# Kernel optimization log

Hardware: AMD Instinct MI355X
Metric: run time of the kernel (lower is better)

Reference implementation:

```python
import jax, jax.numpy as jnp
import numpy as np
import math

EMBED_DIM = 2048
NUM_HEADS = 16
HEAD_DIM = EMBED_DIM // NUM_HEADS  # 128
B, T, S_CACHE = 32, 16, 8192


def setup_inputs() -> dict:
    key = jax.random.key(0)
    ks = jax.random.split(key, 8)
    sc = 0.02
    return {
        "x": jax.random.normal(ks[0], (B, T, EMBED_DIM), dtype=jnp.float32),
        "K_cache": jax.random.normal(ks[1], (B, 1, S_CACHE, HEAD_DIM), dtype=jnp.float32),
        "V_cache": jax.random.normal(ks[2], (B, 1, S_CACHE, HEAD_DIM), dtype=jnp.float32),
        "Wq": jax.random.normal(ks[3], (EMBED_DIM, EMBED_DIM), dtype=jnp.float32) * sc,
        "bq": jnp.zeros((EMBED_DIM,), dtype=jnp.float32),
        "Wk": jax.random.normal(ks[4], (HEAD_DIM, EMBED_DIM), dtype=jnp.float32) * sc,
        "bk": jnp.zeros((HEAD_DIM,), dtype=jnp.float32),
        "Wv": jax.random.normal(ks[5], (HEAD_DIM, EMBED_DIM), dtype=jnp.float32) * sc,
        "bv": jnp.zeros((HEAD_DIM,), dtype=jnp.float32),
        "Wo": jax.random.normal(ks[6], (EMBED_DIM, EMBED_DIM), dtype=jnp.float32) * sc,
        "bo": jnp.zeros((EMBED_DIM,), dtype=jnp.float32),
    }


def reference(x, K_cache, V_cache, Wq, bq, Wk, bk, Wv, bv, Wo, bo):
    b, t, d = x.shape
    # projections (nn.Linear: x @ W.T + b)
    Q = (x @ Wq.T + bq).reshape(b, t, NUM_HEADS, HEAD_DIM).transpose(0, 2, 1, 3)  # [B,H,T,hd]
    K_new = (x @ Wk.T + bk)[:, None, :, :]  # [B,1,T,hd]
    V_new = (x @ Wv.T + bv)[:, None, :, :]
    K = jnp.concatenate([K_cache, K_new], axis=2)  # [B,1,S,hd]
    V = jnp.concatenate([V_cache, V_new], axis=2)
    scale = 1.0 / math.sqrt(HEAD_DIM)
    # shared single KV head broadcast across query heads
    att = jnp.einsum('bhtd,bsd->bhts', Q, K[:, 0]) * scale  # [B,H,T,S]
    att = jax.nn.softmax(att, axis=-1)
    out = jnp.einsum('bhts,bsd->bhtd', att, V[:, 0])  # [B,H,T,hd]
    out = out.transpose(0, 2, 1, 3).reshape(b, t, d)
    out = out @ Wo.T + bo  # dropout is identity in eval mode
    return out
```

## Files before the change

### kernel.cpp

```cpp
#include <hip/hip_runtime.h>
#include <cstdint>

#define EMB 2048
#define NH 16
#define HD 128
#define BB 32
#define TT 16
#define SC 8192
#define ST 8208
#define NS 8
#define QK_SCALE 0.08838834764831845f

typedef __attribute__((ext_vector_type(8))) short short8;
typedef __attribute__((ext_vector_type(4))) float f32x4;

__device__ __forceinline__ ushort f2bf(float f) {
  union { float f; uint32_t u; } v; v.f = f;
  uint32_t u = v.u;
  return (ushort)((u + 0x7FFFu + ((u >> 16) & 1u)) >> 16);
}

typedef __attribute__((address_space(1))) void gas_t;
typedef __attribute__((address_space(3))) void las_t;
__device__ __forceinline__ void gload16(const void* g, void* l) {
  __builtin_amdgcn_global_load_lds((gas_t*)g, (las_t*)l, 16, 0, 0);
}

__global__ __launch_bounds__(256) void prepack(
    const float* __restrict__ x, const float* __restrict__ Wq,
    const float* __restrict__ Wk, const float* __restrict__ Wv,
    const float* __restrict__ Wo, const float* __restrict__ bq,
    const float* __restrict__ bk, const float* __restrict__ bv,
    ushort* __restrict__ xbf, ushort* __restrict__ wqkv,
    ushort* __restrict__ wobf, float* __restrict__ biasq) {
  const int B0 = 262144;
  const int B1 = B0 + 1048576;
  const int B2 = B1 + 65536;
  const int B3 = B2 + 65536;
  const int B4 = B3 + 1048576;
  const int B5 = B4 + 576;
  int stride = gridDim.x * blockDim.x;
  for (int i = blockIdx.x * blockDim.x + threadIdx.x; i < B5; i += stride) {
    const float* src; ushort* dst;
    if (i < B0)      { src = x  + (size_t)i * 4;        dst = xbf  + (size_t)i * 4; }
    else if (i < B1) { src = Wq + (size_t)(i - B0) * 4; dst = wqkv + (size_t)(i - B0) * 4; }
    else if (i < B2) { src = Wk + (size_t)(i - B1) * 4; dst = wqkv + 4194304 + (size_t)(i - B1) * 4; }
    else if (i < B3) { src = Wv + (size_t)(i - B2) * 4; dst = wqkv + 4456448 + (size_t)(i - B2) * 4; }
    else if (i < B4) { src = Wo + (size_t)(i - B3) * 4; dst = wobf + (size_t)(i - B3) * 4; }
    else {
      int j = i - B4;
      const float* bs = (j < 512) ? bq + j * 4 : (j < 544) ? bk + (j - 512) * 4 : bv + (j - 544) * 4;
      float4 f = *(const float4*)bs;
      *(float4*)(biasq + j * 4) = f;
      continue;
    }
    float4 f = *(const float4*)src;
    ushort4 o4;
    o4.x = f2bf(f.x); o4.y = f2bf(f.y); o4.z = f2bf(f.z); o4.w = f2bf(f.w);
    *(ushort4*)dst = o4;
  }
}

__global__ __launch_bounds__(256) void gemm_bt(
    const ushort* __restrict__ A, const ushort* __restrict__ B,
    const float* __restrict__ bias, float* __restrict__ outF,
    ushort* __restrict__ outB, int N, int K, float scale, int scaleLim) {
  __shared__ ushort As[64 * 64];
  __shared__ ushort Bs[128 * 64];
  int tid = threadIdx.x, lane = tid & 63, wid = tid >> 6;
  int wm = wid >> 1, wn = wid & 1;
  int nwg = gridDim.x, bid = blockIdx.x;
  int sw = (bid & 7) * (nwg >> 3) + (bid >> 3);
  const int Mt = 8;
  int nt = sw / Mt, mt = sw % Mt;
  int m0 = mt * 64, n0 = nt * 128;

  f32x4 acc[2][4];
#pragma unroll
  for (int mf = 0; mf < 2; ++mf)
#pragma unroll
    for (int nf = 0; nf < 4; ++nf) acc[mf][nf] = (f32x4){0.f, 0.f, 0.f, 0.f};

  for (int kt = 0; kt < K / 64; ++kt) {
    int kb = kt * 64;
#pragma unroll
    for (int p = 0; p < 2; ++p) {
      int c = wid * 2 + p;
      int row = c * 8 + (lane >> 3);
      int gg = (lane & 7) ^ (row & 7);
      gload16(A + (size_t)(m0 + row) * K + kb + gg * 8, &As[c * 512]);
    }
#pragma unroll
    for (int p = 0; p < 4; ++p) {
      int c = wid * 4 + p;
      int row = c * 8 + (lane >> 3);
      int gg = (lane & 7) ^ (row & 7);
      gload16(B + (size_t)(n0 + row) * K + kb + gg * 8, &Bs[c * 512]);
    }
    __syncthreads();
#pragma unroll
    for (int kk = 0; kk < 2; ++kk) {
      short8 af[2], bf4[4];
#pragma unroll
      for (int mf = 0; mf < 2; ++mf) {
        int r = wm * 32 + mf * 16 + (lane & 15);
        int gg = (kk * 4 + (lane >> 4)) ^ (r & 7);
        af[mf] = *(const short8*)&As[r * 64 + gg * 8];
      }
#pragma unroll
      for (int nf = 0; nf < 4; ++nf) {
        int r = wn * 64 + nf * 16 + (lane & 15);
        int gg = (kk * 4 + (lane >> 4)) ^ (r & 7);
        bf4[nf] = *(const short8*)&Bs[r * 64 + gg * 8];
      }
#pragma unroll
      for (int mf = 0; mf < 2; ++mf)
#pragma unroll
        for (int nf = 0; nf < 4; ++nf)
          acc[mf][nf] = __builtin_amdgcn_mfma_f32_16x16x32_bf16(af[mf], bf4[nf], acc[mf][nf], 0, 0, 0);
    }
    __syncthreads();
  }
#pragma unroll
  for (int mf = 0; mf < 2; ++mf)
#pragma unroll
    for (int nf = 0; nf < 4; ++nf)
#pragma unroll
      for (int r = 0; r < 4; ++r) {
        int gr = m0 + wm * 32 + mf * 16 + (lane >> 4) * 4 + r;
        int gc = n0 + wn * 64 + nf * 16 + (lane & 15);
        float v = acc[mf][nf][r] + bias[gc];
        if (gc < scaleLim) v *= scale;
        if (outB) outB[(size_t)gr * N + gc] = f2bf(v);
        else      outF[(size_t)gr * N + gc] = v;
      }
}

__global__ __launch_bounds__(512) void attn_part(
    const float* __restrict__ Kc, const float* __restrict__ Vc,
    const ushort* __restrict__ Y, float* __restrict__ Op, float* __restrict__ ML) {
  __shared__ ushort Klds[64 * 136];
  __shared__ ushort Vt[128 * 72];
  __shared__ ushort Plds[8][32 * 40];
  int tid = threadIdx.x, lane = tid & 63, wid = tid >> 6;
  int b = blockIdx.y, c = blockIdx.x;
  int s_beg = c * 1024;
  int s_end = (c == NS - 1) ? ST : s_beg + 1024;
  int nsteps = (s_end - s_beg + 63) >> 6;
  int lm = lane & 15, lg = lane >> 4;

  short8 qf[2][4];
#pragma unroll
  for (int mf = 0; mf < 2; ++mf) {
    int qrow = wid * 32 + mf * 16 + lm;
    int h = qrow >> 4, t = qrow & 15;
    const ushort* qp = Y + (size_t)(b * TT + t) * 2304 + h * HD;
#pragma unroll
    for (int ks = 0; ks < 4; ++ks)
      qf[mf][ks] = *(const short8*)(qp + ks * 32 + lg * 8);
  }

  f32x4 o[2][8];
  float mrun[2][4], lrun[2][4];
#pragma unroll
  for (int mf = 0; mf < 2; ++mf) {
#pragma unroll
    for (int nf = 0; nf < 8; ++nf) o[mf][nf] = (f32x4){0.f, 0.f, 0.f, 0.f};
#pragma unroll
    for (int r = 0; r < 4; ++r) { mrun[mf][r] = -1e30f; lrun[mf][r] = 0.f; }
  }

  for (int st = 0; st < nsteps; ++st) {
    int s0 = s_beg + st * 64;
#pragma unroll
    for (int p = 0; p < 4; ++p) {
      int idx = p * 512 + tid;
      int sr = idx >> 5, g4 = idx & 31;
      int s = s0 + sr;
      ushort4 kb4;
      if (s < SC) {
        float4 f = *(const float4*)(Kc + ((size_t)b * SC + s) * HD + g4 * 4);
        kb4.x = f2bf(f.x); kb4.y = f2bf(f.y); kb4.z = f2bf(f.z); kb4.w = f2bf(f.w);
      } else if (s < ST) {
        kb4 = *(const ushort4*)(Y + (size_t)(b * TT + (s - SC)) * 2304 + EMB + g4 * 4);
      } else { kb4.x = kb4.y = kb4.z = kb4.w = 0; }
      *(ushort4*)&Klds[sr * 136 + g4 * 4] = kb4;
    }
    {
      int sb = tid >> 5, db = tid & 31;
      int r0 = sb * 4, d0 = db * 4;
      ushort v0[4], v1[4], v2[4], v3[4];
#pragma unroll
      for (int i = 0; i < 4; ++i) {
        int s = s0 + r0 + i;
        if (s < SC) {
          float4 f = *(const float4*)(Vc + ((size_t)b * SC + s) * HD + d0);
          v0[i] = f2bf(f.x); v1[i] = f2bf(f.y); v2[i] = f2bf(f.z); v3[i] = f2bf(f.w);
        } else if (s < ST) {
          ushort4 t4 = *(const ushort4*)(Y + (size_t)(b * TT + (s - SC)) * 2304 + EMB + HD + d0);
          v0[i] = t4.x; v1[i] = t4.y; v2[i] = t4.z; v3[i] = t4.w;
        } else { v0[i] = v1[i] = v2[i] = v3[i] = 0; }
      }
      ushort4 w;
      w.x = v0[0]; w.y = v0[1]; w.z = v0[2]; w.w = v0[3]; *(ushort4*)&Vt[(d0 + 0) * 72 + r0] = w;
      w.x = v1[0]; w.y = v1[1]; w.z = v1[2]; w.w = v1[3]; *(ushort4*)&Vt[(d0 + 1) * 72 + r0] = w;
      w.x = v2[0]; w.y = v2[1]; w.z = v2[2]; w.w = v2[3]; *(ushort4*)&Vt[(d0 + 2) * 72 + r0] = w;
      w.x = v3[0]; w.y = v3[1]; w.z = v3[2]; w.w = v3[3]; *(ushort4*)&Vt[(d0 + 3) * 72 + r0] = w;
    }
    __syncthreads();

    f32x4 sacc[2][4];
#pragma unroll
    for (int mf = 0; mf < 2; ++mf)
#pragma unroll
      for (int nf = 0; nf < 4; ++nf) sacc[mf][nf] = (f32x4){0.f, 0.f, 0.f, 0.f};
#pragma unroll
    for (int kk = 0; kk < 4; ++kk) {
      short8 kf[4];
#pragma unroll
      for (int nf = 0; nf < 4; ++nf)
        kf[nf] = *(const short8*)&Klds[(nf * 16 + lm) * 136 + kk * 32 + lg * 8];
#pragma unroll
      for (int mf = 0; mf < 2; ++mf)
#pragma unroll
        for (int nf = 0; nf < 4; ++nf)
          sacc[mf][nf] = __builtin_amdgcn_mfma_f32_16x16x32_bf16(qf[mf][kk], kf[nf], sacc[mf][nf], 0, 0, 0);
    }

    if (s0 + 64 > s_end) {
#pragma unroll
      for (int nf = 0; nf < 4; ++nf) {
        int scol = s0 + nf * 16 + lm;
        if (scol >= s_end) {
#pragma unroll
          for (int mf = 0; mf < 2; ++mf)
#pragma unroll
            for (int r = 0; r < 4; ++r) sacc[mf][nf][r] = -1e30f;
        }
      }
    }

#pragma unroll
    for (int mf = 0; mf < 2; ++mf)
#pragma unroll
      for (int r = 0; r < 4; ++r) {
        float mx = fmaxf(fmaxf(sacc[mf][0][r], sacc[mf][1][r]),
                         fmaxf(sacc[mf][2][r], sacc[mf][3][r]));
#pragma unroll
        for (int m = 1; m <= 8; m <<= 1) mx = fmaxf(mx, __shfl_xor(mx, m, 64));
        float mn = fmaxf(mrun[mf][r], mx);
        float scl = __expf(mrun[mf][r] - mn);
        mrun[mf][r] = mn;
        float rs = 0.f;
#pragma unroll
        for (int nf = 0; nf < 4; ++nf) {
          float p = __expf(sacc[mf][nf][r] - mn);
          sacc[mf][nf][r] = p;
          rs += p;
        }
#pragma unroll
        for (int m = 1; m <= 8; m <<= 1) rs += __shfl_xor(rs, m, 64);
        lrun[mf][r] = lrun[mf][r] * scl + rs;
#pragma unroll
        for (int nf = 0; nf < 8; ++nf) o[mf][nf][r] *= scl;
      }

    ushort* pl = Plds[wid];
#pragma unroll
    for (int kh = 0; kh < 2; ++kh) {
#pragma unroll
      for (int mf = 0; mf < 2; ++mf)
#pragma unroll
        for (int nfh = 0; nfh < 2; ++nfh)
#pragma unroll
          for (int r = 0; r < 4; ++r)
            pl[(mf * 16 + lg * 4 + r) * 40 + nfh * 16 + lm] = f2bf(sacc[mf][kh * 2 + nfh][r]);
      short8 pa[2];
#pragma unroll
      for (int mf = 0; mf < 2; ++mf)
        pa[mf] = *(const short8*)&pl[(mf * 16 + lm) * 40 + lg * 8];
#pragma unroll
      for (int nf = 0; nf < 8; ++nf) {
        short8 vb = *(const short8*)&Vt[(nf * 16 + lm) * 72 + kh * 32 + lg * 8];
#pragma unroll
        for (int mf = 0; mf < 2; ++mf)
          o[mf][nf] = __builtin_amdgcn_mfma_f32_16x16x32_bf16(pa[mf], vb, o[mf][nf], 0, 0, 0);
      }
    }
    __syncthreads();
  }

  float* op = Op + (size_t)(b * NS + c) * 256 * HD;
#pragma unroll
  for (int mf = 0; mf < 2; ++mf)
#pragma unroll
    for (int nf = 0; nf < 8; ++nf)
#pragma unroll
      for (int r = 0; r < 4; ++r) {
        int row = wid * 32 + mf * 16 + lg * 4 + r;
        op[(size_t)row * HD + nf * 16 + lm] = o[mf][nf][r];
      }
  if (lm == 0) {
    float* ml = ML + (size_t)(b * NS + c) * 256 * 2;
#pragma unroll
    for (int mf = 0; mf < 2; ++mf)
#pragma unroll
      for (int r = 0; r < 4; ++r) {
        int row = wid * 32 + mf * 16 + lg * 4 + r;
        ml[row * 2] = mrun[mf][r];
        ml[row * 2 + 1] = lrun[mf][r];
      }
  }
}

__global__ __launch_bounds__(256) void attn_reduce(
    const float* __restrict__ Op, const float* __restrict__ ML,
    ushort* __restrict__ abf) {
  int e = blockIdx.x * 256 + threadIdx.x;
  int d = e & 127;
  int r = (e >> 7) & 255;
  int b = e >> 15;
  const float* mlb = ML + (size_t)b * NS * 256 * 2;
  float mv[NS], lv[NS];
  float ms = -1e30f;
#pragma unroll
  for (int c = 0; c < NS; ++c) {
    mv[c] = mlb[(c * 256 + r) * 2];
    lv[c] = mlb[(c * 256 + r) * 2 + 1];
    ms = fmaxf(ms, mv[c]);
  }
  float Ov = 0.f, L = 0.f;
#pragma unroll
  for (int c = 0; c < NS; ++c) {
    float w = __expf(mv[c] - ms);
    L += w * lv[c];
    Ov += w * Op[(((size_t)b * NS + c) * 256 + r) * HD + d];
  }
  float outv = Ov / L;
  int h = r >> 4, t = r & 15;
  abf[(size_t)(b * TT + t) * EMB + h * HD + d] = f2bf(outv);
}

extern "C" void kernel_launch(void* const* d_in, const int* in_sizes, int n_in,
                              void* d_out, int out_size, void* d_ws, size_t ws_size,
                              hipStream_t stream) {
  (void)in_sizes; (void)n_in; (void)out_size; (void)ws_size;
  const float* x  = (const float*)d_in[0];
  const float* Kc = (const float*)d_in[1];
  const float* Vc = (const float*)d_in[2];
  const float* Wq = (const float*)d_in[3];
  const float* bq = (const float*)d_in[4];
  const float* Wk = (const float*)d_in[5];
  const float* bk = (const float*)d_in[6];
  const float* Wv = (const float*)d_in[7];
  const float* bv = (const float*)d_in[8];
  const float* Wo = (const float*)d_in[9];
  const float* bo = (const float*)d_in[10];
  float* out = (float*)d_out;
  char* ws = (char*)d_ws;
  ushort* xbf   = (ushort*)(ws);
  ushort* wqkv  = (ushort*)(ws + 2097152);
  ushort* wobf  = (ushort*)(ws + 11534336);
  ushort* ybf   = (ushort*)(ws + 19922944);
  float*  biasq = (float*) (ws + 22282240);
  float*  Opart = (float*) (ws + 22291456);
  float*  MLp   = (float*) (ws + 55845888);
  ushort* abf   = (ushort*)(ws + 56370176);

  prepack<<<2048, 256, 0, stream>>>(x, Wq, Wk, Wv, Wo, bq, bk, bv, xbf, wqkv, wobf, biasq);
  gemm_bt<<<144, 256, 0, stream>>>(xbf, wqkv, biasq, nullptr, ybf, 2304, 2048, QK_SCALE, 2048);
  attn_part<<<dim3(NS, BB), 512, 0, stream>>>(Kc, Vc, ybf, Opart, MLp);
  attn_reduce<<<4096, 256, 0, stream>>>(Opart, MLp, abf);
  gemm_bt<<<128, 256, 0, stream>>>(abf, wobf, bo, out, nullptr, 2048, 2048, 1.0f, 0);
}
```

Baseline: 471.6 us.

## Software-pipeline attention KV loads via registers and double-buffer GEMM tiles

The attention kernel now prefetches the next 64-row K/V tile into registers while the current tile is converted to bf16, staged in LDS and computed. It uses lgkm-only barriers, raised wave priority around MFMAs, and an XOR-swizzled V transpose buffer. The tail of new K/V rows is handled in a separate final step for the last split. GEMMs shrink to 64x64 tiles with double-buffered LDS and twice the grid size, trading per-block reuse for more parallelism and more register pressure from the prefetch buffers.

```diff
diff --git a/kernel.cpp b/kernel.cpp
--- a/kernel.cpp
+++ b/kernel.cpp
@@ -24,6 +24,13 @@
 typedef __attribute__((address_space(3))) void las_t;
 __device__ __forceinline__ void gload16(const void* g, void* l) {
   __builtin_amdgcn_global_load_lds((gas_t*)g, (las_t*)l, 16, 0, 0);
+}
+
+__device__ __forceinline__ void bar_lgkm() {
+  asm volatile("s_waitcnt lgkmcnt(0)" ::: "memory");
+  __builtin_amdgcn_sched_barrier(0);
+  __builtin_amdgcn_s_barrier();
+  __builtin_amdgcn_sched_barrier(0);
 }
 
 __global__ __launch_bounds__(256) void prepack(
@@ -65,70 +72,74 @@
     const ushort* __restrict__ A, const ushort* __restrict__ B,
     const float* __restrict__ bias, float* __restrict__ outF,
     ushort* __restrict__ outB, int N, int K, float scale, int scaleLim) {
-  __shared__ ushort As[64 * 64];
-  __shared__ ushort Bs[128 * 64];
+  __shared__ ushort As[2][64 * 64];
+  __shared__ ushort Bs[2][64 * 64];
   int tid = threadIdx.x, lane = tid & 63, wid = tid >> 6;
   int wm = wid >> 1, wn = wid & 1;
   int nwg = gridDim.x, bid = blockIdx.x;
   int sw = (bid & 7) * (nwg >> 3) + (bid >> 3);
-  const int Mt = 8;
-  int nt = sw / Mt, mt = sw % Mt;
-  int m0 = mt * 64, n0 = nt * 128;
-
-  f32x4 acc[2][4];
+  int mt = sw & 7, nt = sw >> 3;
+  int m0 = mt * 64, n0 = nt * 64;
+  int lrow = lane >> 3;
+  int gg0 = (lane & 7) ^ (lrow & 7);
+
+  f32x4 acc[2][2];
 #pragma unroll
   for (int mf = 0; mf < 2; ++mf)
 #pragma unroll
-    for (int nf = 0; nf < 4; ++nf) acc[mf][nf] = (f32x4){0.f, 0.f, 0.f, 0.f};
-
-  for (int kt = 0; kt < K / 64; ++kt) {
+    for (int nf = 0; nf < 2; ++nf) acc[mf][nf] = (f32x4){0.f, 0.f, 0.f, 0.f};
+
+  const int KT = K >> 6;
+  auto stage = [&](int buf, int kt) {
     int kb = kt * 64;
-#pragma unroll
-    for (int p = 0; p < 2; ++p) {
-      int c = wid * 2 + p;
-      int row = c * 8 + (lane >> 3);
-      int gg = (lane & 7) ^ (row & 7);
-      gload16(A + (size_t)(m0 + row) * K + kb + gg * 8, &As[c * 512]);
-    }
 #pragma unroll
     for (int p = 0; p < 4; ++p) {
       int c = wid * 4 + p;
-      int row = c * 8 + (lane >> 3);
-      int gg = (lane & 7) ^ (row & 7);
-      gload16(B + (size_t)(n0 + row) * K + kb + gg * 8, &Bs[c * 512]);
-    }
-    __syncthreads();
+      int ca = c & 7;
+      int row = ca * 8 + lrow;
+      const ushort* src = (c < 8) ? A + (size_t)(m0 + row) * K + kb + gg0 * 8
+                                  : B + (size_t)(n0 + row) * K + kb + gg0 * 8;
+      ushort* dst = (c < 8) ? &As[buf][ca * 512] : &Bs[buf][ca * 512];
+      gload16(src, dst);
+    }
+  };
+
+  stage(0, 0);
+  __syncthreads();
+  for (int kt = 0; kt < KT; ++kt) {
+    int cur = kt & 1;
+    if (kt + 1 < KT) stage(cur ^ 1, kt + 1);
 #pragma unroll
     for (int kk = 0; kk < 2; ++kk) {
-      short8 af[2], bf4[4];
+      short8 af[2], bf2[2];
 #pragma unroll
       for (int mf = 0; mf < 2; ++mf) {
         int r = wm * 32 + mf * 16 + (lane & 15);
         int gg = (kk * 4 + (lane >> 4)) ^ (r & 7);
-        af[mf] = *(const short8*)&As[r * 64 + gg * 8];
-      }
-#pragma unroll
-      for (int nf = 0; nf < 4; ++nf) {
-        int r = wn * 64 + nf * 16 + (lane & 15);
+        af[mf] = *(const short8*)&As[cur][r * 64 + gg * 8];
+      }
+#pragma unroll
+      for (int nf = 0; nf < 2; ++nf) {
+        int r = wn * 32 + nf * 16 + (lane & 15);
         int gg = (kk * 4 + (lane >> 4)) ^ (r & 7);
-        bf4[nf] = *(const short8*)&Bs[r * 64 + gg * 8];
+        bf2[nf] = *(const short8*)&Bs[cur][r * 64 + gg * 8];
       }
 #pragma unroll
       for (int mf = 0; mf < 2; ++mf)
 #pragma unroll
-        for (int nf = 0; nf < 4; ++nf)
-          acc[mf][nf] = __builtin_amdgcn_mfma_f32_16x16x32_bf16(af[mf], bf4[nf], acc[mf][nf], 0, 0, 0);
+        for (int nf = 0; nf < 2; ++nf)
+          acc[mf][nf] = __builtin_amdgcn_mfma_f32_16x16x32_bf16(af[mf], bf2[nf], acc[mf][nf], 0, 0, 0);
     }
     __syncthreads();
   }
 #pragma unroll
   for (int mf = 0; mf < 2; ++mf)
 #pragma unroll
-    for (int nf = 0; nf < 4; ++nf)
+    for (int nf = 0; nf < 2; ++nf)
 #pragma unroll
       for (int r = 0; r < 4; ++r) {
         int gr = m0 + wm * 32 + mf * 16 + (lane >> 4) * 4 + r;
-        int gc = n0 + wn * 64 + nf * 16 + (lane & 15);
+        int gc = n0 + wn * 32 + nf * 16 + (lane & 15);
         float v = acc[mf][nf][r] + bias[gc];
         if (gc < scaleLim) v *= scale;
         if (outB) outB[(size_t)gr * N + gc] = f2bf(v);
@@ -140,14 +151,16 @@
     const float* __restrict__ Kc, const float* __restrict__ Vc,
     const ushort* __restrict__ Y, float* __restrict__ Op, float* __restrict__ ML) {
   __shared__ ushort Klds[64 * 136];
-  __shared__ ushort Vt[128 * 72];
+  __shared__ ushort Vt[128 * 64];
   __shared__ ushort Plds[8][32 * 40];
   int tid = threadIdx.x, lane = tid & 63, wid = tid >> 6;
   int b = blockIdx.y, c = blockIdx.x;
   int s_beg = c * 1024;
-  int s_end = (c == NS - 1) ? ST : s_beg + 1024;
-  int nsteps = (s_end - s_beg + 63) >> 6;
   int lm = lane & 15, lg = lane >> 4;
+  int krow = tid >> 5, kcol = tid & 31;
+  int db = tid & 31, sb = tid >> 5;
+  int d0 = db * 4, r0 = sb * 4;
+  int vswz = (db & 7) << 3;
 
   short8 qf[2][4];
 #pragma unroll
@@ -170,45 +183,37 @@
     for (int r = 0; r < 4; ++r) { mrun[mf][r] = -1e30f; lrun[mf][r] = 0.f; }
   }
 
-  for (int st = 0; st < nsteps; ++st) {
-    int s0 = s_beg + st * 64;
+  const float4* K4 = (const float4*)Kc;
+  const float4* V4 = (const float4*)Vc;
+  size_t base4 = (size_t)b * SC * 32;
+
+  auto LOAD = [&](float4 (&kr)[4], float4 (&vr)[4], int s0) {
+#pragma unroll
+    for (int p = 0; p < 4; ++p)
+      kr[p] = K4[base4 + (size_t)(s0 + p * 16 + krow) * 32 + kcol];
+#pragma unroll
+    for (int i = 0; i < 4; ++i)
+      vr[i] = V4[base4 + (size_t)(s0 + r0 + i) * 32 + db];
+  };
+  auto STAGE = [&](const float4 (&kr)[4], const float4 (&vr)[4]) {
 #pragma unroll
     for (int p = 0; p < 4; ++p) {
-      int idx = p * 512 + tid;
-      int sr = idx >> 5, g4 = idx & 31;
-      int s = s0 + sr;
-      ushort4 kb4;
-      if (s < SC) {
-        float4 f = *(const float4*)(Kc + ((size_t)b * SC + s) * HD + g4 * 4);
-        kb4.x = f2bf(f.x); kb4.y = f2bf(f.y); kb4.z = f2bf(f.z); kb4.w = f2bf(f.w);
-      } else if (s < ST) {
-        kb4 = *(const ushort4*)(Y + (size_t)(b * TT + (s - SC)) * 2304 + EMB + g4 * 4);
-      } else { kb4.x = kb4.y = kb4.z = kb4.w = 0; }
-      *(ushort4*)&Klds[sr * 136 + g4 * 4] = kb4;
-    }
-    {
-      int sb = tid >> 5, db = tid & 31;
-      int r0 = sb * 4, d0 = db * 4;
-      ushort v0[4], v1[4], v2[4], v3[4];
-#pragma unroll
-      for (int i = 0; i < 4; ++i) {
-        int s = s0 + r0 + i;
-        if (s < SC) {
-          float4 f = *(const float4*)(Vc + ((size_t)b * SC + s) * HD + d0);
-          v0[i] = f2bf(f.x); v1[i] = f2bf(f.y); v2[i] = f2bf(f.z); v3[i] = f2bf(f.w);
-        } else if (s < ST) {
-          ushort4 t4 = *(const ushort4*)(Y + (size_t)(b * TT + (s - SC)) * 2304 + EMB + HD + d0);
-          v0[i] = t4.x; v1[i] = t4.y; v2[i] = t4.z; v3[i] = t4.w;
-        } else { v0[i] = v1[i] = v2[i] = v3[i] = 0; }
-      }
-      ushort4 w;
-      w.x = v0[0]; w.y = v0[1]; w.z = v0[2]; w.w = v0[3]; *(ushort4*)&Vt[(d0 + 0) * 72 + r0] = w;
-      w.x = v1[0]; w.y = v1[1]; w.z = v1[2]; w.w = v1[3]; *(ushort4*)&Vt[(d0 + 1) * 72 + r0] = w;
-      w.x = v2[0]; w.y = v2[1]; w.z = v2[2]; w.w = v2[3]; *(ushort4*)&Vt[(d0 + 2) * 72 + r0] = w;
-      w.x = v3[0]; w.y = v3[1]; w.z = v3[2]; w.w = v3[3]; *(ushort4*)&Vt[(d0 + 3) * 72 + r0] = w;
-    }
-    __syncthreads();
-
+      ushort4 u;
+      u.x = f2bf(kr[p].x); u.y = f2bf(kr[p].y); u.z = f2bf(kr[p].z); u.w = f2bf(kr[p].w);
+      *(ushort4*)&Klds[(p * 16 + krow) * 136 + kcol * 4] = u;
+    }
+    ushort4 w;
+    w.x = f2bf(vr[0].x); w.y = f2bf(vr[1].x); w.z = f2bf(vr[2].x); w.w = f2bf(vr[3].x);
+    *(ushort4*)&Vt[(d0 + 0) * 64 + (r0 ^ vswz)] = w;
+    w.x = f2bf(vr[0].y); w.y = f2bf(vr[1].y); w.z = f2bf(vr[2].y); w.w = f2bf(vr[3].y);
+    *(ushort4*)&Vt[(d0 + 1) * 64 + (r0 ^ vswz)] = w;
+    w.x = f2bf(vr[0].z); w.y = f2bf(vr[1].z); w.z = f2bf(vr[2].z); w.w = f2bf(vr[3].z);
+    *(ushort4*)&Vt[(d0 + 2) * 64 + (r0 ^ vswz)] = w;
+    w.x = f2bf(vr[0].w); w.y = f2bf(vr[1].w); w.z = f2bf(vr[2].w); w.w = f2bf(vr[3].w);
+    *(ushort4*)&Vt[(d0 + 3) * 64 + (r0 ^ vswz)] = w;
+  };
+
+  auto COMPUTE = [&](int s0, int send) {
     f32x4 sacc[2][4];
 #pragma unroll
     for (int mf = 0; mf < 2; ++mf)
@@ -220,18 +225,19 @@
 #pragma unroll
       for (int nf = 0; nf < 4; ++nf)
         kf[nf] = *(const short8*)&Klds[(nf * 16 + lm) * 136 + kk * 32 + lg * 8];
+      __builtin_amdgcn_s_setprio(1);
 #pragma unroll
       for (int mf = 0; mf < 2; ++mf)
 #pragma unroll
         for (int nf = 0; nf < 4; ++nf)
           sacc[mf][nf] = __builtin_amdgcn_mfma_f32_16x16x32_bf16(qf[mf][kk], kf[nf], sacc[mf][nf], 0, 0, 0);
-    }
-
-    if (s0 + 64 > s_end) {
+      __builtin_amdgcn_s_setprio(0);
+    }
+    if (s0 + 64 > send) {
 #pragma unroll
       for (int nf = 0; nf < 4; ++nf) {
         int scol = s0 + nf * 16 + lm;
-        if (scol >= s_end) {
+        if (scol >= send) {
 #pragma unroll
           for (int mf = 0; mf < 2; ++mf)
 #pragma unroll
@@ -239,7 +245,6 @@
         }
       }
     }
-
 #pragma unroll
     for (int mf = 0; mf < 2; ++mf)
 #pragma unroll
@@ -264,7 +269,6 @@
 #pragma unroll
         for (int nf = 0; nf < 8; ++nf) o[mf][nf][r] *= scl;
       }
-
     ushort* pl = Plds[wid];
 #pragma unroll
     for (int kh = 0; kh < 2; ++kh) {
@@ -281,13 +285,62 @@
         pa[mf] = *(const short8*)&pl[(mf * 16 + lm) * 40 + lg * 8];
 #pragma unroll
       for (int nf = 0; nf < 8; ++nf) {
-        short8 vb = *(const short8*)&Vt[(nf * 16 + lm) * 72 + kh * 32 + lg * 8];
+        int row = nf * 16 + lm;
+        int soff = (kh * 32 + lg * 8) ^ (((row >> 2) & 7) << 3);
+        short8 vb = *(const short8*)&Vt[row * 64 + soff];
+        __builtin_amdgcn_s_setprio(1);
 #pragma unroll
         for (int mf = 0; mf < 2; ++mf)
           o[mf][nf] = __builtin_amdgcn_mfma_f32_16x16x32_bf16(pa[mf], vb, o[mf][nf], 0, 0, 0);
-      }
-    }
-    __syncthreads();
+        __builtin_amdgcn_s_setprio(0);
+      }
+    }
+  };
+
+  float4 kA[4], vA[4], kB[4], vB[4];
+  LOAD(kA, vA, s_beg);
+  for (int st = 0; st < 16; st += 2) {
+    int s1 = s_beg + (st + 1) * 64;
+    LOAD(kB, vB, s1);
+    STAGE(kA, vA);
+    bar_lgkm();
+    COMPUTE(s_beg + st * 64, ST);
+    bar_lgkm();
+    if (st + 2 < 16) LOAD(kA, vA, s_beg + (st + 2) * 64);
+    STAGE(kB, vB);
+    bar_lgkm();
+    COMPUTE(s1, ST);
+    bar_lgkm();
+  }
+
+  if (c == NS - 1) {
+    int s0 = SC;
+#pragma unroll
+    for (int p = 0; p < 4; ++p) {
+      int sr = p * 16 + krow;
+      ushort4 u;
+      if (sr < TT) u = *(const ushort4*)(Y + (size_t)(b * TT + sr) * 2304 + EMB + kcol * 4);
+      else { u.x = u.y = u.z = u.w = 0; }
+      *(ushort4*)&Klds[sr * 136 + kcol * 4] = u;
+    }
+    {
+      ushort v0[4], v1[4], v2[4], v3[4];
+#pragma unroll
+      for (int i = 0; i < 4; ++i) {
+        int sl = r0 + i;
+        if (sl < TT) {
+          ushort4 t4 = *(const ushort4*)(Y + (size_t)(b * TT + sl) * 2304 + EMB + HD + d0);
+          v0[i] = t4.x; v1[i] = t4.y; v2[i] = t4.z; v3[i] = t4.w;
+        } else { v0[i] = v1[i] = v2[i] = v3[i] = 0; }
+      }
+      ushort4 w;
+      w.x = v0[0]; w.y = v0[1]; w.z = v0[2]; w.w = v0[3]; *(ushort4*)&Vt[(d0 + 0) * 64 + (r0 ^ vswz)] = w;
+      w.x = v1[0]; w.y = v1[1]; w.z = v1[2]; w.w = v1[3]; *(ushort4*)&Vt[(d0 + 1) * 64 + (r0 ^ vswz)] = w;
+      w.x = v2[0]; w.y = v2[1]; w.z = v2[2]; w.w = v2[3]; *(ushort4*)&Vt[(d0 + 2) * 64 + (r0 ^ vswz)] = w;
+      w.x = v3[0]; w.y = v3[1]; w.z = v3[2]; w.w = v3[3]; *(ushort4*)&Vt[(d0 + 3) * 64 + (r0 ^ vswz)] = w;
+    }
+    bar_lgkm();
+    COMPUTE(s0, ST);
   }
 
   float* op = Op + (size_t)(b * NS + c) * 256 * HD;
@@ -368,8 +421,8 @@
   ushort* abf   = (ushort*)(ws + 56370176);
 
   prepack<<<2048, 256, 0, stream>>>(x, Wq, Wk, Wv, Wo, bq, bk, bv, xbf, wqkv, wobf, biasq);
-  gemm_bt<<<144, 256, 0, stream>>>(xbf, wqkv, biasq, nullptr, ybf, 2304, 2048, QK_SCALE, 2048);
+  gemm_bt<<<288, 256, 0, stream>>>(xbf, wqkv, biasq, nullptr, ybf, 2304, 2048, QK_SCALE, 2048);
   attn_part<<<dim3(NS, BB), 512, 0, stream>>>(Kc, Vc, ybf, Opart, MLp);
   attn_reduce<<<4096, 256, 0, stream>>>(Opart, MLp, abf);
-  gemm_bt<<<128, 256, 0, stream>>>(abf, wobf, bo, out, nullptr, 2048, 2048, 1.0f, 0);
-}
+  gemm_bt<<<256, 256, 0, stream>>>(abf, wobf, bo, out, nullptr, 2048, 2048, 1.0f, 0);
+}
```

Result: faster. 456.6 us (-3.2%).
